# Kernel optimization log

Measured on AMD Instinct MI355X. Metric: run time of the kernel, lower is better.

The kernel has to match this reference:

```python
import jax, jax.numpy as jnp
import numpy as np

B, S, HID, NH, MAX_TOKENS = 2, 2048, 2048, 16, 2048
HD = HID // NH

def rotate_half(x):
    x1, x2 = x[..., :x.shape[-1] // 2], x[..., x.shape[-1] // 2:]
    return jnp.concatenate((-x2, x1), axis=-1)

def rope_tables():
    inv_freq = 1.0 / (10000.0 ** (jnp.arange(0, HD, 2, dtype=jnp.float32) / HD))
    t = jnp.arange(MAX_TOKENS, dtype=jnp.float32)
    freqs = jnp.outer(t, inv_freq)                       # [T, HD/2]
    emb = jnp.concatenate((freqs, freqs), axis=-1)       # [T, HD]
    return jnp.cos(emb), jnp.sin(emb)

def setup_inputs() -> dict:
    key = jax.random.key(0)
    ks = jax.random.split(key, 5)
    hidden_states = jax.random.normal(ks[0], (B, S, HID), dtype=jnp.float32)
    # additive causal mask [B, 1, S, S]: 0 on/below diag, large negative above
    neg = jnp.finfo(jnp.float32).min
    causal = jnp.where(jnp.tril(jnp.ones((S, S), dtype=bool)), 0.0, neg)
    attention_mask = jnp.broadcast_to(causal[None, None], (B, 1, S, S)).astype(jnp.float32)
    position_ids = jnp.broadcast_to(jnp.arange(S, dtype=jnp.int32), (B, S))
    scale = 1.0 / np.sqrt(HID)
    Wq = jax.random.normal(ks[1], (HID, HID), dtype=jnp.float32) * scale
    Wk = jax.random.normal(ks[2], (HID, HID), dtype=jnp.float32) * scale
    Wv = jax.random.normal(ks[3], (HID, HID), dtype=jnp.float32) * scale
    Wo = jax.random.normal(ks[4], (HID, HID), dtype=jnp.float32) * scale
    return {"hidden_states": hidden_states, "attention_mask": attention_mask,
            "position_ids": position_ids, "Wq": Wq, "Wk": Wk, "Wv": Wv, "Wo": Wo}

def reference(hidden_states, attention_mask, position_ids, Wq, Wk, Wv, Wo):
    b, s, _ = hidden_states.shape
    def proj(W):  # torch Linear: x @ W.T -> [b, H, s, hd]
        return (hidden_states @ W.T).reshape(b, s, NH, HD).transpose(0, 2, 1, 3)
    q, k, v = proj(Wq), proj(Wk), proj(Wv)
    cos_t, sin_t = rope_tables()
    cos = cos_t[position_ids][:, None]   # [b, 1, s, hd]
    sin = sin_t[position_ids][:, None]
    q = q * cos + rotate_half(q) * sin
    k = k * cos + rotate_half(k) * sin
    scores = jnp.einsum('bhqd,bhkd->bhqk', q, k) / np.sqrt(HD)
    scores = jnp.maximum(scores + attention_mask, jnp.finfo(scores.dtype).min)
    attn = jax.nn.softmax(scores.astype(jnp.float32), axis=-1).astype(q.dtype)
    out = jnp.einsum('bhqk,bhkd->bhqd', attn, v)
    out = out.transpose(0, 2, 1, 3).reshape(b, s, HID)
    return out @ Wo.T
```

## Files before the change

### kernel.cpp

```cpp
#include <hip/hip_runtime.h>

#define B_   2
#define S_   2048
#define HID_ 2048
#define NH_  16
#define HD_  128
#define MAXTOK_ 2048

typedef float  f32x4  __attribute__((ext_vector_type(4)));
typedef __bf16 bf16x8 __attribute__((ext_vector_type(8)));

__device__ __forceinline__ unsigned short f2bf(float f) {
  union { float fv; unsigned u; } v; v.fv = f;
  unsigned r = v.u + 0x7FFFu + ((v.u >> 16) & 1u);
  return (unsigned short)(r >> 16);
}
__device__ __forceinline__ float bf2f(unsigned short h) {
  union { unsigned u; float fv; } v; v.u = ((unsigned)h) << 16;
  return v.fv;
}

__device__ __forceinline__ void gload16(const void* g, void* lds) {
  __builtin_amdgcn_global_load_lds(
      (const __attribute__((address_space(1))) void*)g,
      (__attribute__((address_space(3))) void*)lds, 16, 0, 0);
}

#define H4_ (B_ * S_ * HID_ / 4)
#define W4_ (HID_ * HID_ / 4)
__global__ void cast_all(const float* __restrict__ h,  const float* __restrict__ wq,
                         const float* __restrict__ wk, const float* __restrict__ wv,
                         const float* __restrict__ wo,
                         unsigned short* __restrict__ xb,  unsigned short* __restrict__ wqb,
                         unsigned short* __restrict__ wkb, unsigned short* __restrict__ wvb,
                         unsigned short* __restrict__ wob) {
  const int total = H4_ + 4 * W4_;
  int i = blockIdx.x * blockDim.x + threadIdx.x;
  int stride = gridDim.x * blockDim.x;
  for (; i < total; i += stride) {
    const float* src; unsigned short* dst; int j;
    if (i < H4_) { src = h; dst = xb; j = i; }
    else {
      int k = i - H4_, wsel = k >> 20;
      j = k & (W4_ - 1);
      src = (wsel == 0) ? wq : (wsel == 1) ? wk : (wsel == 2) ? wv : wo;
      dst = (wsel == 0) ? wqb : (wsel == 1) ? wkb : (wsel == 2) ? wvb : wob;
    }
    float4 v = ((const float4*)src)[j];
    ushort4 o;
    o.x = f2bf(v.x); o.y = f2bf(v.y); o.z = f2bf(v.z); o.w = f2bf(v.w);
    ((ushort4*)dst)[j] = o;
  }
}

#define QKV_STG(gp, lp, rb) gload16((gp) + (size_t)(rb) * 2048, (lp) + (rb) * 64)

#define QKV_LOADA(MH) do { \
  _Pragma("unroll") \
  for (int mi_ = 0; mi_ < 4; ++mi_) { \
    const char* rp_ = (const char*)Acur + (size_t)((wm + (MH) * 64 + mi_ * 16 + rowq) * 128); \
    af[mi_][0] = *(const bf16x8*)(rp_ + cb0); \
    af[mi_][1] = *(const bf16x8*)(rp_ + cb1); \
  } } while (0)

#define QKV_LOADB(NP) do { \
  _Pragma("unroll") \
  for (int ni_ = 0; ni_ < 2; ++ni_) { \
    const char* rp_ = (const char*)Bcur + (size_t)((wn + (NP) * 32 + ni_ * 16 + rowq) * 128); \
    bfr[ni_][0] = *(const bf16x8*)(rp_ + cb0); \
    bfr[ni_][1] = *(const bf16x8*)(rp_ + cb1); \
  } } while (0)

#define QKV_MFMA(MH, NP) do { \
  _Pragma("unroll") \
  for (int mi_ = 0; mi_ < 4; ++mi_) { \
    _Pragma("unroll") \
    for (int ni_ = 0; ni_ < 2; ++ni_) { \
      f32x4 c_ = acc[(MH) * 4 + mi_][(NP) * 2 + ni_]; \
      c_ = __builtin_amdgcn_mfma_f32_16x16x32_bf16(af[mi_][0], bfr[ni_][0], c_, 0, 0, 0); \
      c_ = __builtin_amdgcn_mfma_f32_16x16x32_bf16(af[mi_][1], bfr[ni_][1], c_, 0, 0, 0); \
      acc[(MH) * 4 + mi_][(NP) * 2 + ni_] = c_; \
    } } } while (0)

#define QKV_BAR    asm volatile("s_barrier" ::: "memory")
#define QKV_VMC2   asm volatile("s_waitcnt vmcnt(2)" ::: "memory")
#define QKV_VMC0   asm volatile("s_waitcnt vmcnt(0)" ::: "memory")

__global__ __launch_bounds__(512, 2)
void gemm_qkv(const unsigned short* __restrict__ A,
              const unsigned short* __restrict__ Bw,
              unsigned short* __restrict__ Qb,
              unsigned short* __restrict__ Kb,
              unsigned short* __restrict__ Vtmp) {
  const int K = HID_;
  const int NT = K / 64;
  __shared__ __align__(16) unsigned short As[2][256 * 64];
  __shared__ __align__(16) unsigned short Bs[2][256 * 64];

  const int tid = threadIdx.x, lane = tid & 63, w = tid >> 6;
  const int n0 = blockIdx.x * 256, m0 = blockIdx.y * 256;
  const int wm = (w >> 2) * 128, wn = (w & 3) * 64;
  const int rowq = lane & 15, klane = lane >> 4;
  const int sw  = ((rowq >> 2) & 1) << 5;
  const int cb0 = (klane * 16) ^ sw;
  const int cb1 = (64 + klane * 16) ^ sw;
  const int srow = tid >> 3;
  const int dc8  = (tid & 7) * 8;
  const int scol = (((tid & 7) * 16) ^ (((srow >> 2) & 1) << 5)) >> 1;

  const unsigned short* Ag = A  + (size_t)(m0 + srow) * K + scol;
  const unsigned short* Bg = Bw + (size_t)(n0 + srow) * K + scol;

  f32x4 acc[8][4];
#pragma unroll
  for (int i = 0; i < 8; ++i)
#pragma unroll
    for (int j = 0; j < 4; ++j)
#pragma unroll
      for (int r = 0; r < 4; ++r) acc[i][j][r] = 0.f;

  bf16x8 af[4][2], bfr[2][2];

  {
    unsigned short* Al = (unsigned short*)&As[0][0] + srow * 64 + dc8;
    unsigned short* Bl = (unsigned short*)&Bs[0][0] + srow * 64 + dc8;
    QKV_STG(Bg, Bl, 0); QKV_STG(Bg, Bl, 64); QKV_STG(Bg, Bl, 128); QKV_STG(Bg, Bl, 192);
    QKV_STG(Ag, Al, 0); QKV_STG(Ag, Al, 128); QKV_STG(Ag, Al, 64); QKV_STG(Ag, Al, 192);
  }
  QKV_VMC2;
  QKV_BAR;

  const unsigned short* Acur = &As[0][0];
  const unsigned short* Bcur = &Bs[0][0];
  unsigned short* Anx = (unsigned short*)&As[1][0];
  unsigned short* Bnx = (unsigned short*)&Bs[1][0];

  for (int t = 0; t < NT - 1; ++t) {
    const int kn = (t + 1) * 64;
    const unsigned short* Agk = Ag + kn;
    const unsigned short* Bgk = Bg + kn;
    unsigned short* Al = Anx + srow * 64 + dc8;
    unsigned short* Bl = Bnx + srow * 64 + dc8;

    QKV_LOADA(0); QKV_LOADB(0);
    QKV_STG(Bgk, Bl, 0); QKV_STG(Bgk, Bl, 64);
    QKV_BAR;
    __builtin_amdgcn_s_setprio(1); QKV_MFMA(0, 0); __builtin_amdgcn_s_setprio(0);
    QKV_VMC2;
    QKV_BAR;
    QKV_LOADA(1);
    QKV_STG(Bgk, Bl, 128); QKV_STG(Bgk, Bl, 192);
    QKV_BAR;
    __builtin_amdgcn_s_setprio(1); QKV_MFMA(1, 0); __builtin_amdgcn_s_setprio(0);
    QKV_BAR;
    QKV_LOADB(1);
    QKV_STG(Agk, Al, 0); QKV_STG(Agk, Al, 128);
    QKV_BAR;
    __builtin_amdgcn_s_setprio(1); QKV_MFMA(1, 1); __builtin_amdgcn_s_setprio(0);
    QKV_BAR;
    QKV_LOADA(0);
    QKV_STG(Agk, Al, 64); QKV_STG(Agk, Al, 192);
    QKV_BAR;
    __builtin_amdgcn_s_setprio(1); QKV_MFMA(0, 1); __builtin_amdgcn_s_setprio(0);
    QKV_VMC2;
    QKV_BAR;

    { const unsigned short* tp = Acur; Acur = Anx; Anx = (unsigned short*)tp; }
    { const unsigned short* tp = Bcur; Bcur = Bnx; Bnx = (unsigned short*)tp; }
  }

  QKV_LOADA(0); QKV_LOADB(0);
  QKV_BAR;
  __builtin_amdgcn_s_setprio(1); QKV_MFMA(0, 0); __builtin_amdgcn_s_setprio(0);
  QKV_VMC0;
  QKV_BAR;
  QKV_LOADA(1);
  QKV_BAR;
  __builtin_amdgcn_s_setprio(1); QKV_MFMA(1, 0); __builtin_amdgcn_s_setprio(0);
  QKV_BAR;
  QKV_LOADB(1);
  QKV_BAR;
  __builtin_amdgcn_s_setprio(1); QKV_MFMA(1, 1); __builtin_amdgcn_s_setprio(0);
  QKV_BAR;
  QKV_LOADA(0);
  QKV_BAR;
  __builtin_amdgcn_s_setprio(1); QKV_MFMA(0, 1); __builtin_amdgcn_s_setprio(0);

  const int lr0 = klane * 4;
#pragma unroll
  for (int mi = 0; mi < 8; ++mi)
#pragma unroll
    for (int ni = 0; ni < 4; ++ni)
#pragma unroll
      for (int r = 0; r < 4; ++r) {
        int r_ = m0 + wm + mi * 16 + lr0 + r;
        int c_ = n0 + wn + ni * 16 + rowq;
        float v = acc[mi][ni][r];
        int b = r_ >> 11, s = r_ & 2047;
        int proj = c_ >> 11, cin = c_ & 2047;
        if (proj == 2) {
          Vtmp[(size_t)(b * S_ + s) * HID_ + cin] = f2bf(v);
        } else {
          int hh = cin >> 7, d = cin & 127;
          unsigned short* dst = (proj == 0) ? Qb : Kb;
          dst[(((size_t)(b * NH_ + hh) * S_ + s) * HD_) + d] = f2bf(v);
        }
      }
}

__global__ __launch_bounds__(256, 2)
void gemm_out(const unsigned short* __restrict__ A,
              const unsigned short* __restrict__ Bw,
              float* __restrict__ Cout) {
  const int N = HID_, K = HID_;
  __shared__ __align__(16) unsigned short As[128 * 32];
  __shared__ __align__(16) unsigned short Bs[128 * 32];
  const int tid = threadIdx.x, lane = tid & 63, w = tid >> 6;
  const int n0 = blockIdx.x * 128, m0 = blockIdx.y * 128;
  const int wm = (w & 1) * 64, wn = (w >> 1) * 64;
  const int rowq = lane & 15;
  const int koff = (lane >> 4) * 8;
  const int lr0 = (lane >> 4) * 4;

  f32x4 acc[4][4];
  for (int i = 0; i < 4; ++i)
    for (int j = 0; j < 4; ++j)
      for (int r = 0; r < 4; ++r) acc[i][j][r] = 0.f;

  for (int k0 = 0; k0 < K; k0 += 32) {
    __syncthreads();
    for (int c = 0; c < 2; ++c) {
      int chunk = (w * 2 + c) * 64 + lane;
      int row = chunk >> 2, cc = chunk & 3;
      gload16(A + (size_t)(m0 + row) * K + k0 + cc * 8, As + (w * 2 + c) * 512);
      gload16(Bw + (size_t)(n0 + row) * K + k0 + cc * 8, Bs + (w * 2 + c) * 512);
    }
    __syncthreads();
    bf16x8 af[4], bfv[4];
    for (int i = 0; i < 4; ++i) {
      af[i]  = *(const bf16x8*)&As[(wm + i * 16 + rowq) * 32 + koff];
      bfv[i] = *(const bf16x8*)&Bs[(wn + i * 16 + rowq) * 32 + koff];
    }
    for (int mi = 0; mi < 4; ++mi)
      for (int ni = 0; ni < 4; ++ni)
        acc[mi][ni] = __builtin_amdgcn_mfma_f32_16x16x32_bf16(af[mi], bfv[ni], acc[mi][ni], 0, 0, 0);
  }

  for (int mi = 0; mi < 4; ++mi)
    for (int ni = 0; ni < 4; ++ni)
      for (int r = 0; r < 4; ++r) {
        int r_ = m0 + wm + mi * 16 + lr0 + r;
        int c_ = n0 + wn + ni * 16 + rowq;
        Cout[(size_t)r_ * N + c_] = acc[mi][ni][r];
      }
}

__global__ void rope_table(float2* __restrict__ tbl) {
  int i = blockIdx.x * blockDim.x + threadIdx.x;
  if (i >= MAXTOK_ * 64) return;
  int p = i >> 6, d = i & 63;
  float f = __expf(-(float)d * (9.210340371976184f / 64.f));
  float sn, cs;
  __sincosf((float)p * f, &sn, &cs);
  tbl[i] = make_float2(cs, sn);
}

#define QSCALE_ 0.12751744f
__global__ __launch_bounds__(256)
void rope_apply(unsigned short* __restrict__ Qb, unsigned short* __restrict__ Kb,
                const int* __restrict__ pos_ids, const float2* __restrict__ tbl) {
  int i = blockIdx.x * blockDim.x + threadIdx.x;
  int d = i & 63, bhs = i >> 6;
  int s = bhs & (S_ - 1);
  int b = bhs >> 15;
  int p = pos_ids[b * S_ + s];
  float2 cssn = tbl[p * 64 + d];
  size_t base = (size_t)bhs * HD_;
  {
    float x1 = bf2f(Qb[base + d]), x2 = bf2f(Qb[base + d + 64]);
    Qb[base + d]      = f2bf((x1 * cssn.x - x2 * cssn.y) * QSCALE_);
    Qb[base + d + 64] = f2bf((x2 * cssn.x + x1 * cssn.y) * QSCALE_);
  }
  {
    float x1 = bf2f(Kb[base + d]), x2 = bf2f(Kb[base + d + 64]);
    Kb[base + d]      = f2bf(x1 * cssn.x - x2 * cssn.y);
    Kb[base + d + 64] = f2bf(x2 * cssn.x + x1 * cssn.y);
  }
}

__global__ __launch_bounds__(256)
void transpose_v(const unsigned short* __restrict__ Vin,
                 unsigned short* __restrict__ Vt) {
  __shared__ unsigned short t[64 * 66];
  const int s0 = blockIdx.x * 64, d0 = blockIdx.y * 64, bh = blockIdx.z;
  const int b = bh >> 4, h = bh & 15;
  for (int it = 0; it < 16; ++it) {
    int lin = it * 256 + threadIdx.x;
    int sl = lin >> 6, dl = lin & 63;
    t[sl * 66 + dl] = Vin[(size_t)(b * S_ + s0 + sl) * HID_ + h * HD_ + d0 + dl];
  }
  __syncthreads();
  for (int it = 0; it < 16; ++it) {
    int lin = it * 256 + threadIdx.x;
    int dl = lin >> 6, sl = lin & 63;
    Vt[((size_t)bh * HD_ + d0 + dl) * S_ + s0 + sl] = t[sl * 66 + dl];
  }
}

#define KS_LD 136
#define VS_LD 72
#define PS_LD 72
__global__ __launch_bounds__(256, 2)
void attn_fused(const unsigned short* __restrict__ Qb,
                const unsigned short* __restrict__ Kb,
                const unsigned short* __restrict__ Vt,
                unsigned short* __restrict__ Ob) {
  __shared__ __align__(16) unsigned short Ks[64 * KS_LD];
  __shared__ __align__(16) unsigned short Vts[128 * VS_LD];
  __shared__ __align__(16) unsigned short Ps[4 * 16 * PS_LD];

  const int tid = threadIdx.x, lane = tid & 63, w = tid >> 6;
  const int bh = blockIdx.x;
  const int qt = (gridDim.y - 1) - blockIdx.y;
  const int q0 = qt * 64;
  const int b = bh >> 4, h = bh & 15;
  const int rowq = lane & 15;
  const int koff = (lane >> 4) * 8;
  const int lr0 = (lane >> 4) * 4;
  const size_t qkbase = (size_t)bh * (S_ * HD_);
  const size_t vbase  = (size_t)bh * (HD_ * S_);

  bf16x8 qf0, qf1, qf2, qf3;
  {
    const unsigned short* qrow = Qb + qkbase + (size_t)(q0 + w * 16 + rowq) * HD_;
    qf0 = *(const bf16x8*)(qrow + 0 * 32 + koff);
    qf1 = *(const bf16x8*)(qrow + 1 * 32 + koff);
    qf2 = *(const bf16x8*)(qrow + 2 * 32 + koff);
    qf3 = *(const bf16x8*)(qrow + 3 * 32 + koff);
  }

  const int krow = tid >> 4, kcol = (tid & 15) * 8;
  const int vrow = tid >> 3, vcol = (tid & 7) * 8;
  const unsigned short* kptr = Kb + qkbase + (size_t)krow * HD_ + kcol;
  const unsigned short* vptr = Vt + vbase + (size_t)vrow * S_ + vcol;

  f32x4 oacc[8];
  for (int i = 0; i < 8; ++i)
    for (int r = 0; r < 4; ++r) oacc[i][r] = 0.f;
  float m_r[4] = {-3e38f, -3e38f, -3e38f, -3e38f};
  float l_r[4] = {0.f, 0.f, 0.f, 0.f};

  const int nkt = qt + 1;

  float4 k0, k1, k2, k3, v0, v1, v2, v3;
  k0 = *(const float4*)(kptr + 0 * 16 * HD_);
  k1 = *(const float4*)(kptr + 1 * 16 * HD_);
  k2 = *(const float4*)(kptr + 2 * 16 * HD_);
  k3 = *(const float4*)(kptr + 3 * 16 * HD_);
  v0 = *(const float4*)(vptr + 0 * 32 * S_);
  v1 = *(const float4*)(vptr + 1 * 32 * S_);
  v2 = *(const float4*)(vptr + 2 * 32 * S_);
  v3 = *(const float4*)(vptr + 3 * 32 * S_);

  for (int kt = 0; kt < nkt; ++kt) {
    __syncthreads();
    *(float4*)&Ks[(krow + 0 * 16) * KS_LD + kcol] = k0;
    *(float4*)&Ks[(krow + 1 * 16) * KS_LD + kcol] = k1;
    *(float4*)&Ks[(krow + 2 * 16) * KS_LD + kcol] = k2;
    *(float4*)&Ks[(krow + 3 * 16) * KS_LD + kcol] = k3;
    *(float4*)&Vts[(vrow + 0 * 32) * VS_LD + vcol] = v0;
    *(float4*)&Vts[(vrow + 1 * 32) * VS_LD + vcol] = v1;
    *(float4*)&Vts[(vrow + 2 * 32) * VS_LD + vcol] = v2;
    *(float4*)&Vts[(vrow + 3 * 32) * VS_LD + vcol] = v3;
    if (kt + 1 < nkt) {
      const unsigned short* kp = kptr + (size_t)(kt + 1) * 64 * HD_;
      k0 = *(const float4*)(kp + 0 * 16 * HD_);
      k1 = *(const float4*)(kp + 1 * 16 * HD_);
      k2 = *(const float4*)(kp + 2 * 16 * HD_);
      k3 = *(const float4*)(kp + 3 * 16 * HD_);
    }
    __syncthreads();

    f32x4 sacc[4];
    for (int n = 0; n < 4; ++n)
      for (int r = 0; r < 4; ++r) sacc[n][r] = 0.f;
#pragma unroll
    for (int n = 0; n < 4; ++n) {
      const unsigned short* krow_p = &Ks[(n * 16 + rowq) * KS_LD + koff];
      sacc[n] = __builtin_amdgcn_mfma_f32_16x16x32_bf16(qf0, *(const bf16x8*)(krow_p + 0 * 32), sacc[n], 0, 0, 0);
      sacc[n] = __builtin_amdgcn_mfma_f32_16x16x32_bf16(qf1, *(const bf16x8*)(krow_p + 1 * 32), sacc[n], 0, 0, 0);
      sacc[n] = __builtin_amdgcn_mfma_f32_16x16x32_bf16(qf2, *(const bf16x8*)(krow_p + 2 * 32), sacc[n], 0, 0, 0);
      sacc[n] = __builtin_amdgcn_mfma_f32_16x16x32_bf16(qf3, *(const bf16x8*)(krow_p + 3 * 32), sacc[n], 0, 0, 0);
    }

    float tmax[4] = {-3e38f, -3e38f, -3e38f, -3e38f};
    if (kt == qt) {
      for (int n = 0; n < 4; ++n) {
        int col = n * 16 + rowq;
        for (int r = 0; r < 4; ++r) {
          int row = w * 16 + lr0 + r;
          float x = (col <= row) ? sacc[n][r] : -1e30f;
          sacc[n][r] = x;
          tmax[r] = fmaxf(tmax[r], x);
        }
      }
    } else {
      for (int n = 0; n < 4; ++n)
        for (int r = 0; r < 4; ++r)
          tmax[r] = fmaxf(tmax[r], sacc[n][r]);
    }
    for (int off = 1; off < 16; off <<= 1)
      for (int r = 0; r < 4; ++r) tmax[r] = fmaxf(tmax[r], __shfl_xor(tmax[r], off));
    float alpha[4];
    for (int r = 0; r < 4; ++r) {
      float mn = fmaxf(m_r[r], tmax[r]);
      alpha[r] = __builtin_amdgcn_exp2f(m_r[r] - mn);
      m_r[r] = mn;
    }
    float rs[4] = {0.f, 0.f, 0.f, 0.f};
    for (int n = 0; n < 4; ++n)
      for (int r = 0; r < 4; ++r) {
        float p = __builtin_amdgcn_exp2f(sacc[n][r] - m_r[r]);
        sacc[n][r] = p;
        rs[r] += p;
      }
    for (int off = 1; off < 16; off <<= 1)
      for (int r = 0; r < 4; ++r) rs[r] += __shfl_xor(rs[r], off);
    for (int r = 0; r < 4; ++r) l_r[r] = l_r[r] * alpha[r] + rs[r];
    for (int nd = 0; nd < 8; ++nd)
      for (int r = 0; r < 4; ++r) oacc[nd][r] *= alpha[r];

    if (kt + 1 < nkt) {
      const unsigned short* vp = vptr + (size_t)(kt + 1) * 64;
      v0 = *(const float4*)(vp + 0 * 32 * S_);
      v1 = *(const float4*)(vp + 1 * 32 * S_);
      v2 = *(const float4*)(vp + 2 * 32 * S_);
      v3 = *(const float4*)(vp + 3 * 32 * S_);
    }

    unsigned short* pw = &Ps[w * 16 * PS_LD];
    for (int n = 0; n < 4; ++n)
      for (int r = 0; r < 4; ++r)
        pw[(lr0 + r) * PS_LD + n * 16 + rowq] = f2bf(sacc[n][r]);

#pragma unroll
    for (int t2 = 0; t2 < 2; ++t2) {
      bf16x8 pa = *(const bf16x8*)&pw[rowq * PS_LD + t2 * 32 + koff];
      for (int nd = 0; nd < 8; ++nd) {
        bf16x8 vb = *(const bf16x8*)&Vts[(nd * 16 + rowq) * VS_LD + t2 * 32 + koff];
        oacc[nd] = __builtin_amdgcn_mfma_f32_16x16x32_bf16(pa, vb, oacc[nd], 0, 0, 0);
      }
    }
  }

  float linv[4];
  for (int r = 0; r < 4; ++r) linv[r] = __builtin_amdgcn_rcpf(l_r[r]);
  for (int nd = 0; nd < 8; ++nd) {
    int col = h * HD_ + nd * 16 + rowq;
    for (int r = 0; r < 4; ++r) {
      int row = q0 + w * 16 + lr0 + r;
      Ob[(size_t)(b * S_ + row) * HID_ + col] = f2bf(oacc[nd][r] * linv[r]);
    }
  }
}

extern "C" void kernel_launch(void* const* d_in, const int* in_sizes, int n_in,
                              void* d_out, int out_size, void* d_ws, size_t ws_size,
                              hipStream_t stream) {
  (void)in_sizes; (void)n_in; (void)out_size; (void)ws_size;
  const float* hidden = (const float*)d_in[0];
  const int* pos = (const int*)d_in[2];
  const float* Wq = (const float*)d_in[3];
  const float* Wk = (const float*)d_in[4];
  const float* Wv = (const float*)d_in[5];
  const float* Wo = (const float*)d_in[6];
  float* out = (float*)d_out;

  char* ws = (char*)d_ws;
  unsigned short* Xb   = (unsigned short*)(ws);
  unsigned short* Wqb  = (unsigned short*)(ws + 16777216);
  unsigned short* Wkb  = (unsigned short*)(ws + 25165824);
  unsigned short* Wvb  = (unsigned short*)(ws + 33554432);
  unsigned short* Wob  = (unsigned short*)(ws + 41943040);
  unsigned short* Qb   = (unsigned short*)(ws + 50331648);
  unsigned short* Kb   = (unsigned short*)(ws + 67108864);
  unsigned short* Vtmp = (unsigned short*)(ws + 83886080);
  unsigned short* Vtb  = (unsigned short*)(ws + 100663296);
  unsigned short* Ob   = Xb;
  float2* tbl          = (float2*)ws;

  cast_all<<<2048, 256, 0, stream>>>(hidden, Wq, Wk, Wv, Wo, Xb, Wqb, Wkb, Wvb, Wob);

  dim3 gq(3 * HID_ / 256, (B_ * S_) / 256);
  gemm_qkv<<<gq, 512, 0, stream>>>(Xb, Wqb, Qb, Kb, Vtmp);

  rope_table<<<(MAXTOK_ * 64) / 256, 256, 0, stream>>>(tbl);
  rope_apply<<<(B_ * NH_ * S_ * 64) / 256, 256, 0, stream>>>(Qb, Kb, pos, tbl);

  dim3 tg(S_ / 64, HD_ / 64, B_ * NH_);
  transpose_v<<<tg, 256, 0, stream>>>(Vtmp, Vtb);

  dim3 ag(B_ * NH_, S_ / 64);
  attn_fused<<<ag, 256, 0, stream>>>(Qb, Kb, Vtb, Ob);

  dim3 go(HID_ / 128, (B_ * S_) / 128);
  gemm_out<<<go, 256, 0, stream>>>(Ob, Wob, out);
}
```

Before: 440.8 us.

## Widen LDS XOR swizzles in QKV and output GEMMs and reorder QKV MFMA phases

Result: faster. 415.2 us (-5.8%).

```diff
diff --git a/kernel.cpp b/kernel.cpp
--- a/kernel.cpp
+++ b/kernel.cpp
@@ -67,8 +67,8 @@
   _Pragma("unroll") \
   for (int ni_ = 0; ni_ < 2; ++ni_) { \
     const char* rp_ = (const char*)Bcur + (size_t)((wn + (NP) * 32 + ni_ * 16 + rowq) * 128); \
-    bfr[ni_][0] = *(const bf16x8*)(rp_ + cb0); \
-    bfr[ni_][1] = *(const bf16x8*)(rp_ + cb1); \
+    bfr[(NP) * 2 + ni_][0] = *(const bf16x8*)(rp_ + cb0); \
+    bfr[(NP) * 2 + ni_][1] = *(const bf16x8*)(rp_ + cb1); \
   } } while (0)
 
 #define QKV_MFMA(MH, NP) do { \
@@ -77,12 +77,13 @@
     _Pragma("unroll") \
     for (int ni_ = 0; ni_ < 2; ++ni_) { \
       f32x4 c_ = acc[(MH) * 4 + mi_][(NP) * 2 + ni_]; \
-      c_ = __builtin_amdgcn_mfma_f32_16x16x32_bf16(af[mi_][0], bfr[ni_][0], c_, 0, 0, 0); \
-      c_ = __builtin_amdgcn_mfma_f32_16x16x32_bf16(af[mi_][1], bfr[ni_][1], c_, 0, 0, 0); \
+      c_ = __builtin_amdgcn_mfma_f32_16x16x32_bf16(af[mi_][0], bfr[(NP) * 2 + ni_][0], c_, 0, 0, 0); \
+      c_ = __builtin_amdgcn_mfma_f32_16x16x32_bf16(af[mi_][1], bfr[(NP) * 2 + ni_][1], c_, 0, 0, 0); \
       acc[(MH) * 4 + mi_][(NP) * 2 + ni_] = c_; \
     } } } while (0)
 
 #define QKV_BAR    asm volatile("s_barrier" ::: "memory")
+#define QKV_VMC4   asm volatile("s_waitcnt vmcnt(4)" ::: "memory")
 #define QKV_VMC2   asm volatile("s_waitcnt vmcnt(2)" ::: "memory")
 #define QKV_VMC0   asm volatile("s_waitcnt vmcnt(0)" ::: "memory")
 
@@ -101,12 +102,12 @@
   const int n0 = blockIdx.x * 256, m0 = blockIdx.y * 256;
   const int wm = (w >> 2) * 128, wn = (w & 3) * 64;
   const int rowq = lane & 15, klane = lane >> 4;
-  const int sw  = ((rowq >> 2) & 1) << 5;
+  const int sw  = (rowq & 7) << 4;
   const int cb0 = (klane * 16) ^ sw;
-  const int cb1 = (64 + klane * 16) ^ sw;
+  const int cb1 = ((klane + 4) * 16) ^ sw;
   const int srow = tid >> 3;
   const int dc8  = (tid & 7) * 8;
-  const int scol = (((tid & 7) * 16) ^ (((srow >> 2) & 1) << 5)) >> 1;
+  const int scol = (((tid & 7) * 16) ^ ((srow & 7) << 4)) >> 1;
 
   const unsigned short* Ag = A  + (size_t)(m0 + srow) * K + scol;
   const unsigned short* Bg = Bw + (size_t)(n0 + srow) * K + scol;
@@ -119,7 +120,7 @@
 #pragma unroll
       for (int r = 0; r < 4; ++r) acc[i][j][r] = 0.f;
 
-  bf16x8 af[4][2], bfr[2][2];
+  bf16x8 af[4][2], bfr[4][2];
 
   {
     unsigned short* Al = (unsigned short*)&As[0][0] + srow * 64 + dc8;
@@ -146,22 +147,21 @@
     QKV_STG(Bgk, Bl, 0); QKV_STG(Bgk, Bl, 64);
     QKV_BAR;
     __builtin_amdgcn_s_setprio(1); QKV_MFMA(0, 0); __builtin_amdgcn_s_setprio(0);
-    QKV_VMC2;
+    QKV_BAR;
+    QKV_LOADB(1);
+    QKV_STG(Bgk, Bl, 128); QKV_STG(Bgk, Bl, 192);
+    QKV_BAR;
+    __builtin_amdgcn_s_setprio(1); QKV_MFMA(0, 1); __builtin_amdgcn_s_setprio(0);
+    QKV_VMC4;
     QKV_BAR;
     QKV_LOADA(1);
-    QKV_STG(Bgk, Bl, 128); QKV_STG(Bgk, Bl, 192);
+    QKV_STG(Agk, Al, 0); QKV_STG(Agk, Al, 128);
+    QKV_BAR;
+    __builtin_amdgcn_s_setprio(1); QKV_MFMA(1, 1); __builtin_amdgcn_s_setprio(0);
+    QKV_BAR;
+    QKV_STG(Agk, Al, 64); QKV_STG(Agk, Al, 192);
     QKV_BAR;
     __builtin_amdgcn_s_setprio(1); QKV_MFMA(1, 0); __builtin_amdgcn_s_setprio(0);
-    QKV_BAR;
-    QKV_LOADB(1);
-    QKV_STG(Agk, Al, 0); QKV_STG(Agk, Al, 128);
-    QKV_BAR;
-    __builtin_amdgcn_s_setprio(1); QKV_MFMA(1, 1); __builtin_amdgcn_s_setprio(0);
-    QKV_BAR;
-    QKV_LOADA(0);
-    QKV_STG(Agk, Al, 64); QKV_STG(Agk, Al, 192);
-    QKV_BAR;
-    __builtin_amdgcn_s_setprio(1); QKV_MFMA(0, 1); __builtin_amdgcn_s_setprio(0);
     QKV_VMC2;
     QKV_BAR;
 
@@ -172,19 +172,17 @@
   QKV_LOADA(0); QKV_LOADB(0);
   QKV_BAR;
   __builtin_amdgcn_s_setprio(1); QKV_MFMA(0, 0); __builtin_amdgcn_s_setprio(0);
+  QKV_BAR;
+  QKV_LOADB(1);
+  QKV_BAR;
+  __builtin_amdgcn_s_setprio(1); QKV_MFMA(0, 1); __builtin_amdgcn_s_setprio(0);
   QKV_VMC0;
   QKV_BAR;
   QKV_LOADA(1);
   QKV_BAR;
+  __builtin_amdgcn_s_setprio(1); QKV_MFMA(1, 1); __builtin_amdgcn_s_setprio(0);
+  QKV_BAR;
   __builtin_amdgcn_s_setprio(1); QKV_MFMA(1, 0); __builtin_amdgcn_s_setprio(0);
-  QKV_BAR;
-  QKV_LOADB(1);
-  QKV_BAR;
-  __builtin_amdgcn_s_setprio(1); QKV_MFMA(1, 1); __builtin_amdgcn_s_setprio(0);
-  QKV_BAR;
-  QKV_LOADA(0);
-  QKV_BAR;
-  __builtin_amdgcn_s_setprio(1); QKV_MFMA(0, 1); __builtin_amdgcn_s_setprio(0);
 
   const int lr0 = klane * 4;
 #pragma unroll
@@ -219,8 +217,9 @@
   const int n0 = blockIdx.x * 128, m0 = blockIdx.y * 128;
   const int wm = (w & 1) * 64, wn = (w >> 1) * 64;
   const int rowq = lane & 15;
-  const int koff = (lane >> 4) * 8;
-  const int lr0 = (lane >> 4) * 4;
+  const int klane = lane >> 4;
+  const int ko = ((klane ^ ((rowq >> 1) & 3)) * 8);
+  const int lr0 = klane * 4;
 
   f32x4 acc[4][4];
   for (int i = 0; i < 4; ++i)
@@ -232,14 +231,15 @@
     for (int c = 0; c < 2; ++c) {
       int chunk = (w * 2 + c) * 64 + lane;
       int row = chunk >> 2, cc = chunk & 3;
-      gload16(A + (size_t)(m0 + row) * K + k0 + cc * 8, As + (w * 2 + c) * 512);
-      gload16(Bw + (size_t)(n0 + row) * K + k0 + cc * 8, Bs + (w * 2 + c) * 512);
+      int sc = (cc ^ ((row >> 1) & 3)) * 8;
+      gload16(A + (size_t)(m0 + row) * K + k0 + sc, As + (w * 2 + c) * 512);
+      gload16(Bw + (size_t)(n0 + row) * K + k0 + sc, Bs + (w * 2 + c) * 512);
     }
     __syncthreads();
     bf16x8 af[4], bfv[4];
     for (int i = 0; i < 4; ++i) {
-      af[i]  = *(const bf16x8*)&As[(wm + i * 16 + rowq) * 32 + koff];
-      bfv[i] = *(const bf16x8*)&Bs[(wn + i * 16 + rowq) * 32 + koff];
+      af[i]  = *(const bf16x8*)&As[(wm + i * 16 + rowq) * 32 + ko];
+      bfv[i] = *(const bf16x8*)&Bs[(wn + i * 16 + rowq) * 32 + ko];
     }
     for (int mi = 0; mi < 4; ++mi)
       for (int ni = 0; ni < 4; ++ni)
```
